# Optimization experiments

Hardware: AMD Instinct MI355X
Metric: run time of the kernel (lower is better)

Reference implementation:

```python
import jax, jax.numpy as jnp
import numpy as np

RATE = 22050.0 / 256.0  # audio_target_rate from the torch source
SIZES = [2.23147392 * RATE, 2.62519274 * RATE, 3.74199546 * RATE,
         5.78800454 * RATE, 8.02371882 * RATE, float('inf')]
WEIGHT = 1.0
EPS = 1e-7


def _giou_1d(a, b):
    # a, b: [P, 2] intervals (start, end); elementwise 1-D GIoU
    inter = jnp.clip(jnp.minimum(a[:, 1], b[:, 1]) - jnp.maximum(a[:, 0], b[:, 0]), 0.0)
    union = (a[:, 1] - a[:, 0]) + (b[:, 1] - b[:, 0]) - inter
    iou = inter / (union + EPS)
    enclose = jnp.maximum(a[:, 1], b[:, 1]) - jnp.minimum(a[:, 0], b[:, 0])
    return iou - (enclose - union) / (enclose + EPS)


def setup_inputs() -> dict:
    key = jax.random.key(0)
    ks = jax.random.split(key, 4)
    B, N = 4, 32
    L0 = 131072  # frames at the finest level
    levels = 6
    anchors = {f"anchors_l{i}": (jnp.arange(L0 >> i, dtype=jnp.float32) + 0.5) * (2.0 ** i)
               for i in range(levels)}
    A = sum(int(v.shape[0]) for v in anchors.values())  # 258048
    # GT intervals: all rows belong to class 0 (matches class_id filter in the source)
    starts = jax.random.uniform(ks[0], (B, N), minval=0.0, maxval=float(L0) - 2000.0)
    lens = jax.random.uniform(ks[1], (B, N), minval=50.0, maxval=1500.0)
    annotations = jnp.stack([starts, starts + lens, jnp.zeros((B, N))], axis=-1).astype(jnp.float32)
    # Predicted intervals for every anchor
    c = jax.random.uniform(ks[2], (B, A), minval=0.0, maxval=float(L0))
    w = jax.random.uniform(ks[3], (B, A), minval=10.0, maxval=2000.0)
    regressions = jnp.stack([c - 0.5 * w, c + 0.5 * w], axis=-1).astype(jnp.float32)
    out = {"regressions": regressions, "annotations": annotations, "class_id": 0}
    out.update(anchors)
    return out


def reference(regressions, annotations, anchors_l0, anchors_l1, anchors_l2,
              anchors_l3, anchors_l4, anchors_l5, class_id):
    anchors_list = [anchors_l0, anchors_l1, anchors_l2, anchors_l3, anchors_l4, anchors_l5]
    all_pts = jnp.concatenate(anchors_list)  # [A]

    def per_sample(reg, ann):
        # ann: [N, 3]; inputs guarantee every row has class == class_id and is valid
        order = jnp.argsort(ann[:, 1] - ann[:, 0])  # sort GT by length ascending
        ann = ann[order]
        s, e = ann[:, 0:1], ann[:, 1:2]  # [N,1]
        pos_parts, nl_parts, nr_parts = [], [], []
        for i, pts in enumerate(anchors_list):
            l = pts[None, :] - s            # [N, A_i]
            r = e - pts[None, :]            # [N, A_i]
            in_gt = (l >= 0.0) & (r >= 0.0)
            m = jnp.maximum(l, r)
            lower = SIZES[i - 1] if i > 0 else 0.0
            cand = in_gt & (m >= lower) & (m < SIZES[i])
            pos_parts.append(cand.any(axis=0))
            amax = jnp.argmax(cand, axis=0)  # first True per anchor (0 if none)
            inv = 1.0 / (2.0 ** i)           # normalize l*/r* by 2**level
            nl_parts.append(jnp.take_along_axis(l, amax[None, :], axis=0)[0] * inv)
            nr_parts.append(jnp.take_along_axis(r, amax[None, :], axis=0)[0] * inv)
        pos = jnp.concatenate(pos_parts)   # [A] bool
        nl = jnp.concatenate(nl_parts)     # [A]
        nr = jnp.concatenate(nr_parts)     # [A]
        # decoded normalized target boxes around the anchor points
        boxes = jnp.stack([all_pts - nl, all_pts + nr], axis=1)  # [A, 2]
        giou = jnp.clip(_giou_1d(boxes, reg[:, :2]), -1.0, 1.0)
        loss = 1.0 - giou
        posf = pos.astype(loss.dtype)
        # masked mean over positive anchors (torch indexes by boolean mask then .mean())
        return jnp.sum(loss * posf) / jnp.maximum(jnp.sum(posf), 1.0) * WEIGHT

    return jax.vmap(per_sample)(regressions, annotations)  # [B] per-sample losses
```

## Files before the change

kernel.cpp:

```cpp
#include <hip/hip_runtime.h>

#define EPS_F 1e-7f
#define NN 32
#define PT 4

__global__ __launch_bounds__(256) void rl_main(
    const float* __restrict__ reg,
    const float* __restrict__ ann,
    int c0, int A, int gx,
    float* __restrict__ ws)
{
    const int b = blockIdx.y;
    const int t = threadIdx.x;
    __shared__ float2 sh_se[NN];
    __shared__ float2 sh_band[8];

    if (t < 6) {
        const float sz[7] = {
            0.0f,
            (float)(2.23147392 * (22050.0 / 256.0)),
            (float)(2.62519274 * (22050.0 / 256.0)),
            (float)(3.74199546 * (22050.0 / 256.0)),
            (float)(5.78800454 * (22050.0 / 256.0)),
            (float)(8.02371882 * (22050.0 / 256.0)),
            __builtin_inff()
        };
        sh_band[t] = make_float2(sz[t], sz[t + 1]);
    }

    if (t < NN) {
        const float* an = ann + (size_t)b * (size_t)NN * 3;
        const float s0 = an[t * 3 + 0];
        const float e0 = an[t * 3 + 1];
        const float len = e0 - s0;
        int rank = 0;
#pragma unroll
        for (int j = 0; j < NN; ++j) {
            const float lj = __shfl(len, j, 64);
            rank += (lj < len) || (lj == len && j < t);
        }
        sh_se[rank] = make_float2(s0, e0);
    }
    __syncthreads();

    const int log2c0 = 31 - __clz(c0);
    const int twoc0  = 2 * c0;
    const int clzoff = 31 - log2c0;
    float pt_[PT], lo_[PT], hi_[PT], inv_[PT];
    const int base = blockIdx.x * (256 * PT) + t;
#pragma unroll
    for (int k = 0; k < PT; ++k) {
        const int a   = base + k * 256;
        const int lvl = __clz(twoc0 - 1 - a) - clzoff;
        const int loc = a - twoc0 + (twoc0 >> lvl);
        const float scale = __int_as_float((127 + lvl) << 23);
        inv_[k] = __int_as_float((127 - lvl) << 23);
        pt_[k]  = ((float)loc + 0.5f) * scale;
        const float2 band = sh_band[lvl];
        lo_[k] = band.x;
        hi_[k] = band.y;
    }

    float bl_[PT], br_[PT];
    bool  fnd_[PT];
    {
        const float2 se0 = sh_se[0];
#pragma unroll
        for (int k = 0; k < PT; ++k) {
            bl_[k] = pt_[k] - se0.x;
            br_[k] = se0.y - pt_[k];
            fnd_[k] = false;
        }
    }
    for (int n = NN - 1; n >= 0; --n) {
        const float2 se = sh_se[n];
#pragma unroll
        for (int k = 0; k < PT; ++k) {
            const float l = pt_[k] - se.x;
            const float r = se.y - pt_[k];
            const float m = fmaxf(l, r);
            const float u = fminf(fminf(l, r), m - lo_[k]);
            const bool cand = (u >= 0.0f) & (m < hi_[k]);
            bl_[k] = cand ? l : bl_[k];
            br_[k] = cand ? r : br_[k];
            fnd_[k] |= cand;
        }
    }

    float loss_sum = 0.0f, pos_sum = 0.0f;
#pragma unroll
    for (int k = 0; k < PT; ++k) {
        const int a = base + k * 256;
        const float pt = pt_[k];
        const float b0 = pt - bl_[k] * inv_[k];
        const float b1 = pt + br_[k] * inv_[k];
        const float2 g = *(const float2*)(reg + ((size_t)b * A + a) * 2);
        const float inter = fmaxf(fminf(b1, g.y) - fmaxf(b0, g.x), 0.0f);
        const float uni = (b1 - b0) + (g.y - g.x) - inter;
        const float iou = inter * __builtin_amdgcn_rcpf(uni + EPS_F);
        const float enc = fmaxf(b1, g.y) - fminf(b0, g.x);
        float giou = iou - (enc - uni) * __builtin_amdgcn_rcpf(enc + EPS_F);
        giou = fminf(fmaxf(giou, -1.0f), 1.0f);
        if (fnd_[k]) { loss_sum += 1.0f - giou; pos_sum += 1.0f; }
    }

    for (int o = 32; o > 0; o >>= 1) {
        loss_sum += __shfl_down(loss_sum, o, 64);
        pos_sum  += __shfl_down(pos_sum,  o, 64);
    }
    __shared__ float red_l[4], red_p[4];
    const int wave = t >> 6;
    if ((t & 63) == 0) { red_l[wave] = loss_sum; red_p[wave] = pos_sum; }
    __syncthreads();
    if (t == 0) {
        float Ls = red_l[0] + red_l[1] + red_l[2] + red_l[3];
        float Ps = red_p[0] + red_p[1] + red_p[2] + red_p[3];
        float* slot = ws + ((size_t)b * gx + blockIdx.x) * 2;
        slot[0] = Ls;
        slot[1] = Ps;
    }
}

__global__ void rl_fin(const float* __restrict__ ws, float* __restrict__ out,
                       int gx) {
    const int b = threadIdx.x >> 6;
    const int lane = threadIdx.x & 63;
    float Ls = 0.0f, Ps = 0.0f;
    for (int i = lane; i < gx; i += 64) {
        const float2 p = *(const float2*)(ws + ((size_t)b * gx + i) * 2);
        Ls += p.x;
        Ps += p.y;
    }
    for (int o = 32; o > 0; o >>= 1) {
        Ls += __shfl_down(Ls, o, 64);
        Ps += __shfl_down(Ps, o, 64);
    }
    if (lane == 0) out[b] = Ls / fmaxf(Ps, 1.0f);
}

extern "C" void kernel_launch(void* const* d_in, const int* in_sizes, int n_in,
                              void* d_out, int out_size, void* d_ws, size_t ws_size,
                              hipStream_t stream) {
    const float* reg = (const float*)d_in[0];
    const float* ann = (const float*)d_in[1];
    const int c0 = in_sizes[3];
    const int A = in_sizes[3] + in_sizes[4] + in_sizes[5] +
                  in_sizes[6] + in_sizes[7] + in_sizes[8];
    const int B = out_size;

    const int threads = 256;
    int gx = (A + threads * PT - 1) / (threads * PT);
    if (gx < 1) gx = 1;
    dim3 grid(gx, B);
    float* ws = (float*)d_ws;
    rl_main<<<grid, threads, 0, stream>>>(reg, ann, c0, A, gx, ws);
    rl_fin<<<1, 64 * B, 0, stream>>>(ws, (float*)d_out, gx);
}
```

Baseline: 83.04 us.

## Iterate only anchors inside each GT interval instead of scanning all anchors

The dense per-anchor scan over all 258K anchors and 32 GT intervals is replaced with one block per (GT, sample). Each block computes, per level, the index ranges of anchors whose max(l,r) falls in that level's size band, evaluates only those, and counts an anchor only if no earlier (shorter) GT also claims it. Non-positive anchors contribute nothing to the masked mean, so the regressions for them are never read. The cost is fewer threads (128 blocks), uneven work per block, a serial scan over earlier GTs for each candidate, and reliance on the analytic range bounds plus margin being exact.

```diff
diff --git a/kernel.cpp b/kernel.cpp
--- a/kernel.cpp
+++ b/kernel.cpp
@@ -2,31 +2,29 @@
 
 #define EPS_F 1e-7f
 #define NN 32
-#define PT 4
+#define MARGIN 3
 
-__global__ __launch_bounds__(256) void rl_main(
+__global__ __launch_bounds__(256) void rl_sparse(
     const float* __restrict__ reg,
     const float* __restrict__ ann,
-    int c0, int A, int gx,
+    int c0, int A,
     float* __restrict__ ws)
 {
+    const int n = blockIdx.x;
     const int b = blockIdx.y;
     const int t = threadIdx.x;
+
     __shared__ float2 sh_se[NN];
-    __shared__ float2 sh_band[8];
 
-    if (t < 6) {
-        const float sz[7] = {
-            0.0f,
-            (float)(2.23147392 * (22050.0 / 256.0)),
-            (float)(2.62519274 * (22050.0 / 256.0)),
-            (float)(3.74199546 * (22050.0 / 256.0)),
-            (float)(5.78800454 * (22050.0 / 256.0)),
-            (float)(8.02371882 * (22050.0 / 256.0)),
-            __builtin_inff()
-        };
-        sh_band[t] = make_float2(sz[t], sz[t + 1]);
-    }
+    const float sz[7] = {
+        0.0f,
+        (float)(2.23147392 * (22050.0 / 256.0)),
+        (float)(2.62519274 * (22050.0 / 256.0)),
+        (float)(3.74199546 * (22050.0 / 256.0)),
+        (float)(5.78800454 * (22050.0 / 256.0)),
+        (float)(8.02371882 * (22050.0 / 256.0)),
+        __builtin_inff()
+    };
 
     if (t < NN) {
         const float* an = ann + (size_t)b * (size_t)NN * 3;
@@ -43,65 +41,70 @@
     }
     __syncthreads();
 
-    const int log2c0 = 31 - __clz(c0);
-    const int twoc0  = 2 * c0;
-    const int clzoff = 31 - log2c0;
-    float pt_[PT], lo_[PT], hi_[PT], inv_[PT];
-    const int base = blockIdx.x * (256 * PT) + t;
-#pragma unroll
-    for (int k = 0; k < PT; ++k) {
-        const int a   = base + k * 256;
-        const int lvl = __clz(twoc0 - 1 - a) - clzoff;
-        const int loc = a - twoc0 + (twoc0 >> lvl);
+    const float s = sh_se[n].x;
+    const float e = sh_se[n].y;
+    const float mid   = 0.5f * (s + e);
+    const float halfL = 0.5f * (e - s);
+
+    const int twoc0 = 2 * c0;
+    float loss_sum = 0.0f, pos_sum = 0.0f;
+
+    for (int lvl = 0; lvl < 6; ++lvl) {
+        const float lo = sz[lvl];
+        const float hi = sz[lvl + 1];
+        const int   cnt  = c0 >> lvl;
+        const int   aoff = twoc0 - (twoc0 >> lvl);
         const float scale = __int_as_float((127 + lvl) << 23);
-        inv_[k] = __int_as_float((127 - lvl) << 23);
-        pt_[k]  = ((float)loc + 0.5f) * scale;
-        const float2 band = sh_band[lvl];
-        lo_[k] = band.x;
-        hi_[k] = band.y;
-    }
+        const float inv   = __int_as_float((127 - lvl) << 23);
 
-    float bl_[PT], br_[PT];
-    bool  fnd_[PT];
-    {
-        const float2 se0 = sh_se[0];
-#pragma unroll
-        for (int k = 0; k < PT; ++k) {
-            bl_[k] = pt_[k] - se0.x;
-            br_[k] = se0.y - pt_[k];
-            fnd_[k] = false;
+        const float dlo = fmaxf(lo - halfL, 0.0f);
+        const float dhi = hi - halfL;
+        const float prl = fmaxf(mid + dlo, s);
+        const float prh = fminf(mid + dhi, e);
+        const float pll = fmaxf(mid - dhi, s);
+        const float plh = fminf(mid - dlo, e);
+
+        int r0 = (int)floorf(prl * inv - 0.5f) - MARGIN;
+        int r1 = (int)floorf(prh * inv - 0.5f) + MARGIN;
+        int l0 = (int)floorf(pll * inv - 0.5f) - MARGIN;
+        int l1 = (int)floorf(plh * inv - 0.5f) + MARGIN;
+        r0 = max(r0, 0); r1 = min(r1, cnt - 1);
+        l0 = max(l0, 0); l1 = min(l1, cnt - 1);
+        if (r1 >= r0) l1 = min(l1, r0 - 1);
+        const int lenL = max(l1 - l0 + 1, 0);
+        const int lenR = max(r1 - r0 + 1, 0);
+        const int total = lenL + lenR;
+
+        for (int j = t; j < total; j += 256) {
+            const int loc = (j < lenL) ? (l0 + j) : (r0 + (j - lenL));
+            const float pt = ((float)loc + 0.5f) * scale;
+            const float l = pt - s;
+            const float r = e - pt;
+            const float m = fmaxf(l, r);
+            if (!((fminf(l, r) >= 0.0f) & (m >= lo) & (m < hi))) continue;
+            bool first = true;
+            for (int n2 = 0; n2 < n; ++n2) {
+                const float2 o = sh_se[n2];
+                const float l2 = pt - o.x;
+                const float r2 = o.y - pt;
+                const float m2 = fmaxf(l2, r2);
+                if ((fminf(l2, r2) >= 0.0f) & (m2 >= lo) & (m2 < hi)) {
+                    first = false; break;
+                }
+            }
+            if (!first) continue;
+            const float b0 = pt - l * inv;
+            const float b1 = pt + r * inv;
+            const float2 g = ((const float2*)reg)[(size_t)b * A + (aoff + loc)];
+            const float inter = fmaxf(fminf(b1, g.y) - fmaxf(b0, g.x), 0.0f);
+            const float uni = (b1 - b0) + (g.y - g.x) - inter;
+            const float iou = inter * __builtin_amdgcn_rcpf(uni + EPS_F);
+            const float enc = fmaxf(b1, g.y) - fminf(b0, g.x);
+            float giou = iou - (enc - uni) * __builtin_amdgcn_rcpf(enc + EPS_F);
+            giou = fminf(fmaxf(giou, -1.0f), 1.0f);
+            loss_sum += 1.0f - giou;
+            pos_sum  += 1.0f;
         }
-    }
-    for (int n = NN - 1; n >= 0; --n) {
-        const float2 se = sh_se[n];
-#pragma unroll
-        for (int k = 0; k < PT; ++k) {
-            const float l = pt_[k] - se.x;
-            const float r = se.y - pt_[k];
-            const float m = fmaxf(l, r);
-            const float u = fminf(fminf(l, r), m - lo_[k]);
-            const bool cand = (u >= 0.0f) & (m < hi_[k]);
-            bl_[k] = cand ? l : bl_[k];
-            br_[k] = cand ? r : br_[k];
-            fnd_[k] |= cand;
-        }
-    }
-
-    float loss_sum = 0.0f, pos_sum = 0.0f;
-#pragma unroll
-    for (int k = 0; k < PT; ++k) {
-        const int a = base + k * 256;
-        const float pt = pt_[k];
-        const float b0 = pt - bl_[k] * inv_[k];
-        const float b1 = pt + br_[k] * inv_[k];
-        const float2 g = *(const float2*)(reg + ((size_t)b * A + a) * 2);
-        const float inter = fmaxf(fminf(b1, g.y) - fmaxf(b0, g.x), 0.0f);
-        const float uni = (b1 - b0) + (g.y - g.x) - inter;
-        const float iou = inter * __builtin_amdgcn_rcpf(uni + EPS_F);
-        const float enc = fmaxf(b1, g.y) - fminf(b0, g.x);
-        float giou = iou - (enc - uni) * __builtin_amdgcn_rcpf(enc + EPS_F);
-        giou = fminf(fmaxf(giou, -1.0f), 1.0f);
-        if (fnd_[k]) { loss_sum += 1.0f - giou; pos_sum += 1.0f; }
     }
 
     for (int o = 32; o > 0; o >>= 1) {
@@ -115,7 +118,7 @@
     if (t == 0) {
         float Ls = red_l[0] + red_l[1] + red_l[2] + red_l[3];
         float Ps = red_p[0] + red_p[1] + red_p[2] + red_p[3];
-        float* slot = ws + ((size_t)b * gx + blockIdx.x) * 2;
+        float* slot = ws + ((size_t)b * NN + n) * 2;
         slot[0] = Ls;
         slot[1] = Ps;
     }
@@ -148,11 +151,8 @@
                   in_sizes[6] + in_sizes[7] + in_sizes[8];
     const int B = out_size;
 
-    const int threads = 256;
-    int gx = (A + threads * PT - 1) / (threads * PT);
-    if (gx < 1) gx = 1;
-    dim3 grid(gx, B);
     float* ws = (float*)d_ws;
-    rl_main<<<grid, threads, 0, stream>>>(reg, ann, c0, A, gx, ws);
-    rl_fin<<<1, 64 * B, 0, stream>>>(ws, (float*)d_out, gx);
+    dim3 grid(NN, B);
+    rl_sparse<<<grid, 256, 0, stream>>>(reg, ann, c0, A, ws);
+    rl_fin<<<1, 64 * B, 0, stream>>>(ws, (float*)d_out, NN);
 }
```

After: 80.49 us. -3.1%, faster.
